# Performance work log

Measured on AMD Instinct MI355X. Metric: run time of the kernel, lower is better.

The kernel has to match this reference:

```python
import jax, jax.numpy as jnp
import numpy as np

N_EXPERTS = 8
TOPK = 2


def setup_inputs() -> dict:
    key = jax.random.key(0)
    k1, k2, k3, k4 = jax.random.split(key, 4)
    B, T, D, H, E = 2, 2048, 1024, 4096, N_EXPERTS
    s = 1.0 / np.sqrt(D)
    return {
        "x": jax.random.normal(k1, (B, T, D), dtype=jnp.float32),
        "W_gate": jax.random.normal(k2, (E, D), dtype=jnp.float32) * s,
        "W_fc": jax.random.normal(k3, (E, H, D), dtype=jnp.float32) * s,
        "W_proj": jax.random.normal(k4, (E, D, H), dtype=jnp.float32) * (1.0 / np.sqrt(H)),
    }


def reference(x, W_gate, W_fc, W_proj):
    B, T, D = x.shape
    E = W_gate.shape[0]
    N = B * T
    xf = x.reshape(N, D)

    # gating
    gate_logits = xf @ W_gate.T                       # [N, E]
    gate_probs = jax.nn.softmax(gate_logits, axis=-1)
    rw, eidx = jax.lax.top_k(gate_probs, TOPK)        # [N, K]
    rw = rw / jnp.sum(rw, axis=-1, keepdims=True)

    # exact dispatch: out[n] = sum_k rw[n,k] * MLP_{eidx[n,k]}(x[n])
    # loop over the small fixed expert count; each expert processes all tokens,
    # masked-combined by its per-token routing weight (same math as index_add dispatch).
    out = jnp.zeros_like(xf)
    for e in range(E):
        we = jnp.sum(jnp.where(eidx == e, rw, 0.0), axis=-1)     # [N]
        h = jnp.square(jax.nn.relu(xf @ W_fc[e].T))              # relu(x)^2, [N, H]
        out = out + (h @ W_proj[e].T) * we[:, None]

    # load-balance loss
    ones = jnp.ones((N * TOPK,), dtype=gate_probs.dtype)
    counts = jax.ops.segment_sum(ones, eidx.reshape(-1), num_segments=E)
    expert_freq = counts / N
    balance_loss = jnp.sum(gate_probs.mean(axis=0) * jax.lax.stop_gradient(expert_freq)) * E

    return out.reshape(B, T, D), balance_loss
```

## Files before the change

kernel.cpp:

```cpp
#include <hip/hip_runtime.h>
#include <hip/hip_bf16.h>
#include <math.h>

#define N_TOK 4096
#define D_DIM 1024
#define H_DIM 4096
#define E_NUM 8
#define NSLOT (N_TOK * 2)

typedef short bf16x8 __attribute__((ext_vector_type(8)));
typedef float f32x4 __attribute__((ext_vector_type(4)));


__device__ __forceinline__ unsigned short f2bf(float f) {
  unsigned int u = __float_as_uint(f);
  u += 0x7FFFu + ((u >> 16) & 1u);
  return (unsigned short)(u >> 16);
}

__device__ __forceinline__ void gld_lds16(const void* g, void* l) {
  __builtin_amdgcn_global_load_lds(
      (__attribute__((address_space(1))) void*)(g),
      (__attribute__((address_space(3))) void*)(l), 16, 0, 0);
}


__global__ void init_ctrl(int* p) { p[threadIdx.x] = 0; }

__global__ void cvt_f32_bf16(const float* __restrict__ src,
                             unsigned short* __restrict__ dst, int n4) {
  int i = blockIdx.x * blockDim.x + threadIdx.x;
  if (i >= n4) return;
  float4 v = ((const float4*)src)[i];
  ushort4 o;
  o.x = f2bf(v.x); o.y = f2bf(v.y); o.z = f2bf(v.z); o.w = f2bf(v.w);
  ((ushort4*)dst)[i] = o;
}

__global__ void zero_f32(float* __restrict__ p, int n4) {
  int i = blockIdx.x * blockDim.x + threadIdx.x;
  if (i < n4) ((float4*)p)[i] = make_float4(0.f, 0.f, 0.f, 0.f);
}


__global__ void gating_kernel(const float* __restrict__ x,
                              const float* __restrict__ wg,
                              float* __restrict__ probs,
                              int* __restrict__ eidx,
                              float* __restrict__ rw) {
  __shared__ float4 wg_lds[2048];
  const int t = threadIdx.x;
  const int lane = t & 63;
  const int wave = t >> 6;

#pragma unroll
  for (int j = 0; j < 8; ++j)
    wg_lds[t + 256 * j] = ((const float4*)wg)[t + 256 * j];
  __syncthreads();

#pragma unroll
  for (int j = 0; j < 4; ++j) {
    const int n = blockIdx.x * 16 + wave * 4 + j;
    const float4* xr = (const float4*)(x + (size_t)n * D_DIM);

    float acc[E_NUM];
#pragma unroll
    for (int e = 0; e < E_NUM; ++e) acc[e] = 0.f;

#pragma unroll
    for (int i = 0; i < 4; ++i) {
      float4 xv = xr[lane + 64 * i];
#pragma unroll
      for (int e = 0; e < E_NUM; ++e) {
        float4 wv = wg_lds[e * 256 + lane + 64 * i];
        acc[e] += xv.x * wv.x + xv.y * wv.y + xv.z * wv.z + xv.w * wv.w;
      }
    }
#pragma unroll
    for (int m = 1; m < 64; m <<= 1) {
#pragma unroll
      for (int e = 0; e < E_NUM; ++e) acc[e] += __shfl_xor(acc[e], m, 64);
    }

    float mx = acc[0];
#pragma unroll
    for (int e = 1; e < E_NUM; ++e) mx = fmaxf(mx, acc[e]);
    float p[E_NUM], s = 0.f;
#pragma unroll
    for (int e = 0; e < E_NUM; ++e) { p[e] = __expf(acc[e] - mx); s += p[e]; }
    float inv = 1.f / s;

    if (lane < E_NUM) probs[(size_t)n * E_NUM + lane] = p[lane] * inv;

    if (lane == 0) {
      int i1 = 0;
#pragma unroll
      for (int e = 1; e < E_NUM; ++e) if (p[e] > p[i1]) i1 = e;
      int i2 = (i1 == 0) ? 1 : 0;
#pragma unroll
      for (int e = 0; e < E_NUM; ++e)
        if (e != i1 && p[e] > p[i2]) i2 = e;
      float p1 = p[i1], p2 = p[i2];
      float wsum = 1.f / (p1 + p2);
      eidx[n] = i1 | (i2 << 8);
      rw[2 * n] = p1 * wsum;
      rw[2 * n + 1] = p2 * wsum;
    }
  }
}

__global__ void reduce_route(const float* __restrict__ probs,
                             const int* __restrict__ eidx,
                             int* __restrict__ counts,
                             int* __restrict__ offsets,
                             float* __restrict__ loss) {
  const int t = threadIdx.x;
  float4 part = make_float4(0.f, 0.f, 0.f, 0.f);
  for (int j = 0; j < 32; ++j) {
    float4 v = ((const float4*)probs)[t + 256 * j];
    part.x += v.x; part.y += v.y; part.z += v.z; part.w += v.w;
  }
  int cnt[E_NUM];
#pragma unroll
  for (int e = 0; e < E_NUM; ++e) cnt[e] = 0;
  for (int j = 0; j < 16; ++j) {
    int pk = eidx[t + 256 * j];
    int e1 = pk & 255, e2 = pk >> 8;
#pragma unroll
    for (int e = 0; e < E_NUM; ++e) cnt[e] += (e1 == e) + (e2 == e);
  }

  __shared__ float redf[256 * E_NUM];
  __shared__ int redi[256 * E_NUM];
  const int eb = (t & 1) * 4;
#pragma unroll
  for (int e = 0; e < E_NUM; ++e) { redf[t * E_NUM + e] = 0.f; redi[t * E_NUM + e] = cnt[e]; }
  redf[t * E_NUM + eb + 0] = part.x;
  redf[t * E_NUM + eb + 1] = part.y;
  redf[t * E_NUM + eb + 2] = part.z;
  redf[t * E_NUM + eb + 3] = part.w;
  __syncthreads();
  for (int s = 128; s > 0; s >>= 1) {
    if (t < s) {
#pragma unroll
      for (int e = 0; e < E_NUM; ++e) {
        redf[t * E_NUM + e] += redf[(t + s) * E_NUM + e];
        redi[t * E_NUM + e] += redi[(t + s) * E_NUM + e];
      }
    }
    __syncthreads();
  }
  if (t == 0) {
    int o = 0;
    float L = 0.f;
    for (int e = 0; e < E_NUM; ++e) {
      int c = redi[e];
      counts[e] = c;
      offsets[e] = o;
      o += c;
      L += redf[e] * (float)c;
    }
    loss[0] = L * (float)E_NUM / ((float)N_TOK * (float)N_TOK);
  }
}

__global__ void scatter_kernel(const int* __restrict__ eidx, const float* __restrict__ rw,
                               const int* __restrict__ offsets, int* __restrict__ cursor,
                               int* __restrict__ tok_id, float* __restrict__ tok_w) {
  __shared__ int lcnt[E_NUM];
  __shared__ int lbase[E_NUM];
  const int t = threadIdx.x;
  const int n = blockIdx.x * 256 + t;
  if (t < E_NUM) lcnt[t] = 0;
  __syncthreads();
  int pk = eidx[n];
  int e1 = pk & 255, e2 = pk >> 8;
  int p1 = atomicAdd(&lcnt[e1], 1);
  int p2 = atomicAdd(&lcnt[e2], 1);
  __syncthreads();
  if (t < E_NUM) lbase[t] = atomicAdd(&cursor[t], lcnt[t]);
  __syncthreads();
  int d1 = offsets[e1] + lbase[e1] + p1;
  tok_id[d1] = n; tok_w[d1] = rw[2 * n];
  int d2 = offsets[e2] + lbase[e2] + p2;
  tok_id[d2] = n; tok_w[d2] = rw[2 * n + 1];
}


__launch_bounds__(256, 2)
__global__ void gemm_fc(const unsigned short* __restrict__ xb,
                        const unsigned short* __restrict__ wfc,
                        const int* __restrict__ tok_id,
                        const int* __restrict__ counts,
                        const int* __restrict__ offsets,
                        unsigned short* __restrict__ hbuf) {
  const int e = blockIdx.z;
  const int cnt = counts[e];
  const int mtile = blockIdx.y;
  if (mtile * 128 >= cnt) return;
  const int ntile = blockIdx.x;
  const int off = offsets[e];

  __shared__ __align__(16) unsigned short As[128 * 64];
  __shared__ __align__(16) unsigned short Bs[128 * 64];

  const int t = threadIdx.x;
  const int lane = t & 63;
  const int wave = t >> 6;
  const int wm = (wave >> 1) * 64;
  const int wn = (wave & 1) * 64;
  const int srow = t >> 3;
  const int seg = (t & 7) ^ (srow & 7);

  const unsigned short* aptr[4];
  const unsigned short* bptr[4];
#pragma unroll
  for (int p = 0; p < 4; ++p) {
    int r = mtile * 128 + p * 32 + srow;
    r = (r < cnt) ? r : (cnt - 1);
    int tok = tok_id[off + r];
    aptr[p] = xb + (size_t)tok * D_DIM + seg * 8;
    int br = ntile * 128 + p * 32 + srow;
    bptr[p] = wfc + ((size_t)e * H_DIM + br) * D_DIM + seg * 8;
  }

  f32x4 acc[4][4];
#pragma unroll
  for (int i = 0; i < 4; ++i)
#pragma unroll
    for (int j = 0; j < 4; ++j) acc[i][j] = (f32x4){0.f, 0.f, 0.f, 0.f};

  const int frow_a = wm + (lane & 15);
  const int frow_b = wn + (lane & 15);
  const int q = lane >> 4;
  const int csw = lane & 7;

  for (int k0 = 0; k0 < D_DIM; k0 += 64) {
#pragma unroll
    for (int p = 0; p < 4; ++p) {
      gld_lds16(aptr[p] + k0, &As[p * 2048 + t * 8]);
      gld_lds16(bptr[p] + k0, &Bs[p * 2048 + t * 8]);
    }
    __syncthreads();
#pragma unroll
    for (int kk = 0; kk < 64; kk += 32) {
      const int ca = ((((kk >> 3) + q) ^ csw) << 3);
      bf16x8 af[4], bfr[4];
#pragma unroll
      for (int i = 0; i < 4; ++i)
        af[i] = *(const bf16x8*)&As[(frow_a + i * 16) * 64 + ca];
#pragma unroll
      for (int j = 0; j < 4; ++j)
        bfr[j] = *(const bf16x8*)&Bs[(frow_b + j * 16) * 64 + ca];
#pragma unroll
      for (int i = 0; i < 4; ++i)
#pragma unroll
        for (int j = 0; j < 4; ++j)
          acc[i][j] = __builtin_amdgcn_mfma_f32_16x16x32_bf16(af[i], bfr[j], acc[i][j], 0, 0, 0);
    }
    __syncthreads();
  }

  const int lm = (lane >> 4) * 4;
  const int ln = lane & 15;
#pragma unroll
  for (int i = 0; i < 4; ++i) {
#pragma unroll
    for (int r = 0; r < 4; ++r) {
      int m = mtile * 128 + wm + i * 16 + lm + r;
      if (m < cnt) {
        size_t rowbase = (size_t)(off + m) * H_DIM + ntile * 128 + wn;
#pragma unroll
        for (int j = 0; j < 4; ++j) {
          float v = acc[i][j][r];
          v = v > 0.f ? v * v : 0.f;
          hbuf[rowbase + j * 16 + ln] = f2bf(v);
        }
      }
    }
  }
}

__launch_bounds__(256, 2)
__global__ void gemm_proj(const unsigned short* __restrict__ hbuf,
                          const unsigned short* __restrict__ wproj,
                          const int* __restrict__ tok_id,
                          const float* __restrict__ tok_w,
                          const int* __restrict__ counts,
                          const int* __restrict__ offsets,
                          float* __restrict__ out) {
  const int e = blockIdx.z >> 1;
  const int kbase = (blockIdx.z & 1) * (H_DIM / 2);
  const int cnt = counts[e];
  const int mtile = blockIdx.y;
  if (mtile * 128 >= cnt) return;
  const int ntile = blockIdx.x;
  const int off = offsets[e];

  __shared__ __align__(16) unsigned short As[128 * 64];
  __shared__ __align__(16) unsigned short Bs[128 * 64];

  const int t = threadIdx.x;
  const int lane = t & 63;
  const int wave = t >> 6;
  const int wm = (wave >> 1) * 64;
  const int wn = (wave & 1) * 64;
  const int srow = t >> 3;
  const int seg = (t & 7) ^ (srow & 7);

  const unsigned short* aptr[4];
  const unsigned short* bptr[4];
#pragma unroll
  for (int p = 0; p < 4; ++p) {
    int r = mtile * 128 + p * 32 + srow;
    r = (r < cnt) ? r : (cnt - 1);
    aptr[p] = hbuf + (size_t)(off + r) * H_DIM + seg * 8;
    int br = ntile * 128 + p * 32 + srow;
    bptr[p] = wproj + ((size_t)e * D_DIM + br) * H_DIM + seg * 8;
  }

  f32x4 acc[4][4];
#pragma unroll
  for (int i = 0; i < 4; ++i)
#pragma unroll
    for (int j = 0; j < 4; ++j) acc[i][j] = (f32x4){0.f, 0.f, 0.f, 0.f};

  const int frow_a = wm + (lane & 15);
  const int frow_b = wn + (lane & 15);
  const int q = lane >> 4;
  const int csw = lane & 7;

  for (int k0 = kbase; k0 < kbase + H_DIM / 2; k0 += 64) {
#pragma unroll
    for (int p = 0; p < 4; ++p) {
      gld_lds16(aptr[p] + k0, &As[p * 2048 + t * 8]);
      gld_lds16(bptr[p] + k0, &Bs[p * 2048 + t * 8]);
    }
    __syncthreads();
#pragma unroll
    for (int kk = 0; kk < 64; kk += 32) {
      const int ca = ((((kk >> 3) + q) ^ csw) << 3);
      bf16x8 af[4], bfr[4];
#pragma unroll
      for (int i = 0; i < 4; ++i)
        af[i] = *(const bf16x8*)&As[(frow_a + i * 16) * 64 + ca];
#pragma unroll
      for (int j = 0; j < 4; ++j)
        bfr[j] = *(const bf16x8*)&Bs[(frow_b + j * 16) * 64 + ca];
#pragma unroll
      for (int i = 0; i < 4; ++i)
#pragma unroll
        for (int j = 0; j < 4; ++j)
          acc[i][j] = __builtin_amdgcn_mfma_f32_16x16x32_bf16(af[i], bfr[j], acc[i][j], 0, 0, 0);
    }
    __syncthreads();
  }

  const int lm = (lane >> 4) * 4;
  const int ln = lane & 15;
#pragma unroll
  for (int i = 0; i < 4; ++i) {
#pragma unroll
    for (int r = 0; r < 4; ++r) {
      int m = mtile * 128 + wm + i * 16 + lm + r;
      if (m < cnt) {
        int slot = off + m;
        float w = tok_w[slot];
        float* orow = out + (size_t)tok_id[slot] * D_DIM + ntile * 128 + wn;
#pragma unroll
        for (int j = 0; j < 4; ++j)
          atomicAdd(&orow[j * 16 + ln], acc[i][j][r] * w);
      }
    }
  }
}


extern "C" void kernel_launch(void* const* d_in, const int* in_sizes, int n_in,
                              void* d_out, int out_size, void* d_ws, size_t ws_size,
                              hipStream_t stream) {
  (void)in_sizes; (void)n_in; (void)out_size; (void)ws_size;
  const float* x = (const float*)d_in[0];
  const float* wg = (const float*)d_in[1];
  const float* wfc = (const float*)d_in[2];
  const float* wproj = (const float*)d_in[3];
  float* out = (float*)d_out;
  char* ws = (char*)d_ws;

  int* counts = (int*)(ws + 0);
  int* cursor = (int*)(ws + 64);
  int* offsets = (int*)(ws + 128);
  int* eidx = (int*)(ws + 256);
  float* rw = (float*)(ws + 16640);
  int* tok_id = (int*)(ws + 49408);
  float* tok_w = (float*)(ws + 82176);
  float* probs = (float*)(ws + 114944);
  unsigned short* xb = (unsigned short*)(ws + 246016);
  unsigned short* wfcb = (unsigned short*)(ws + 8634624);
  unsigned short* wpjb = (unsigned short*)(ws + 75743488);
  unsigned short* hbuf = (unsigned short*)(ws + 142852352);

  hipLaunchKernelGGL(init_ctrl, dim3(1), dim3(64), 0, stream, (int*)ws);
  hipLaunchKernelGGL(cvt_f32_bf16, dim3(32768), dim3(256), 0, stream, wfc, wfcb, 8388608);
  hipLaunchKernelGGL(cvt_f32_bf16, dim3(32768), dim3(256), 0, stream, wproj, wpjb, 8388608);
  hipLaunchKernelGGL(cvt_f32_bf16, dim3(4096), dim3(256), 0, stream, x, xb, 1048576);
  hipLaunchKernelGGL(zero_f32, dim3(4096), dim3(256), 0, stream, out, 1048576);
  hipLaunchKernelGGL(gating_kernel, dim3(256), dim3(256), 0, stream, x, wg, probs, eidx, rw);
  hipLaunchKernelGGL(reduce_route, dim3(1), dim3(256), 0, stream, probs, eidx, counts, offsets, out + 4194304);
  hipLaunchKernelGGL(scatter_kernel, dim3(16), dim3(256), 0, stream, eidx, rw, offsets, cursor, tok_id, tok_w);
  hipLaunchKernelGGL(gemm_fc, dim3(32, 32, 8), dim3(256), 0, stream, xb, wfcb, tok_id, counts, offsets, hbuf);
  hipLaunchKernelGGL(gemm_proj, dim3(8, 32, 16), dim3(256), 0, stream, hbuf, wpjb, tok_id, tok_w, counts, offsets, out);
}
```

Before: 563.2 us.

## Triple-buffer LDS pipeline with 256x128 tiles in expert GEMMs

```diff
diff --git a/kernel.cpp b/kernel.cpp
--- a/kernel.cpp
+++ b/kernel.cpp
@@ -187,7 +187,7 @@
 }
 
 
-__launch_bounds__(256, 2)
+__launch_bounds__(512, 2)
 __global__ void gemm_fc(const unsigned short* __restrict__ xb,
                         const unsigned short* __restrict__ wfc,
                         const int* __restrict__ tok_id,
@@ -197,32 +197,32 @@
   const int e = blockIdx.z;
   const int cnt = counts[e];
   const int mtile = blockIdx.y;
-  if (mtile * 128 >= cnt) return;
+  if (mtile * 256 >= cnt) return;
   const int ntile = blockIdx.x;
   const int off = offsets[e];
 
-  __shared__ __align__(16) unsigned short As[128 * 64];
-  __shared__ __align__(16) unsigned short Bs[128 * 64];
+  __shared__ __align__(16) unsigned short lds[3 * 24576];
 
   const int t = threadIdx.x;
   const int lane = t & 63;
   const int wave = t >> 6;
   const int wm = (wave >> 1) * 64;
   const int wn = (wave & 1) * 64;
+
   const int srow = t >> 3;
   const int seg = (t & 7) ^ (srow & 7);
 
   const unsigned short* aptr[4];
-  const unsigned short* bptr[4];
+  const unsigned short* bptr[2];
 #pragma unroll
   for (int p = 0; p < 4; ++p) {
-    int r = mtile * 128 + p * 32 + srow;
+    int r = mtile * 256 + p * 64 + srow;
     r = (r < cnt) ? r : (cnt - 1);
-    int tok = tok_id[off + r];
-    aptr[p] = xb + (size_t)tok * D_DIM + seg * 8;
-    int br = ntile * 128 + p * 32 + srow;
-    bptr[p] = wfc + ((size_t)e * H_DIM + br) * D_DIM + seg * 8;
-  }
+    aptr[p] = xb + (size_t)tok_id[off + r] * D_DIM + seg * 8;
+  }
+#pragma unroll
+  for (int p = 0; p < 2; ++p)
+    bptr[p] = wfc + ((size_t)e * H_DIM + ntile * 128 + p * 64 + srow) * D_DIM + seg * 8;
 
   f32x4 acc[4][4];
 #pragma unroll
@@ -230,58 +230,96 @@
 #pragma unroll
     for (int j = 0; j < 4; ++j) acc[i][j] = (f32x4){0.f, 0.f, 0.f, 0.f};
 
-  const int frow_a = wm + (lane & 15);
-  const int frow_b = wn + (lane & 15);
+  const int fr = lane & 15;
   const int q = lane >> 4;
   const int csw = lane & 7;
-
-  for (int k0 = 0; k0 < D_DIM; k0 += 64) {
-#pragma unroll
-    for (int p = 0; p < 4; ++p) {
-      gld_lds16(aptr[p] + k0, &As[p * 2048 + t * 8]);
-      gld_lds16(bptr[p] + k0, &Bs[p * 2048 + t * 8]);
-    }
-    __syncthreads();
-#pragma unroll
-    for (int kk = 0; kk < 64; kk += 32) {
-      const int ca = ((((kk >> 3) + q) ^ csw) << 3);
-      bf16x8 af[4], bfr[4];
-#pragma unroll
-      for (int i = 0; i < 4; ++i)
-        af[i] = *(const bf16x8*)&As[(frow_a + i * 16) * 64 + ca];
-#pragma unroll
-      for (int j = 0; j < 4; ++j)
-        bfr[j] = *(const bf16x8*)&Bs[(frow_b + j * 16) * 64 + ca];
-#pragma unroll
-      for (int i = 0; i < 4; ++i)
-#pragma unroll
-        for (int j = 0; j < 4; ++j)
-          acc[i][j] = __builtin_amdgcn_mfma_f32_16x16x32_bf16(af[i], bfr[j], acc[i][j], 0, 0, 0);
-    }
-    __syncthreads();
+  const int c0 = ((q ^ csw) << 3);
+  const int c1 = (((q + 4) ^ csw) << 3);
+
+  const int NK = D_DIM / 64;
+
+#pragma unroll
+  for (int p = 0; p < 4; ++p) gld_lds16(aptr[p], &lds[p * 4096 + t * 8]);
+#pragma unroll
+  for (int p = 0; p < 2; ++p) gld_lds16(bptr[p], &lds[16384 + p * 4096 + t * 8]);
+#pragma unroll
+  for (int p = 0; p < 4; ++p) gld_lds16(aptr[p] + 64, &lds[24576 + p * 4096 + t * 8]);
+#pragma unroll
+  for (int p = 0; p < 2; ++p) gld_lds16(bptr[p] + 64, &lds[24576 + 16384 + p * 4096 + t * 8]);
+  asm volatile("s_waitcnt vmcnt(6)" ::: "memory");
+  __builtin_amdgcn_s_barrier();
+
+  int sb = 0;
+  for (int kt = 0; kt < NK; ++kt) {
+    int stS = sb + 2 * 24576; if (stS >= 3 * 24576) stS -= 3 * 24576;
+    const unsigned short* Ab = &lds[sb + (wm + fr) * 64];
+    const unsigned short* Bb = &lds[sb + 16384 + (wn + fr) * 64];
+    const int kof = (kt + 2) * 64;
+    bf16x8 a_[4], b_[4];
+
+#pragma unroll
+    for (int m = 0; m < 4; ++m) a_[m] = *(const bf16x8*)(Ab + m * 1024 + c0);
+#pragma unroll
+    for (int n = 0; n < 4; ++n) b_[n] = *(const bf16x8*)(Bb + n * 1024 + c0);
+    if (kt + 2 < NK) {
+      gld_lds16(aptr[0] + kof, &lds[stS + t * 8]);
+      gld_lds16(aptr[1] + kof, &lds[stS + 4096 + t * 8]);
+      gld_lds16(aptr[2] + kof, &lds[stS + 8192 + t * 8]);
+    }
+    __builtin_amdgcn_s_barrier();
+    __builtin_amdgcn_s_setprio(1);
+#pragma unroll
+    for (int m = 0; m < 4; ++m)
+#pragma unroll
+      for (int n = 0; n < 4; ++n)
+        acc[m][n] = __builtin_amdgcn_mfma_f32_16x16x32_bf16(a_[m], b_[n], acc[m][n], 0, 0, 0);
+    __builtin_amdgcn_s_setprio(0);
+    __builtin_amdgcn_s_barrier();
+
+#pragma unroll
+    for (int m = 0; m < 4; ++m) a_[m] = *(const bf16x8*)(Ab + m * 1024 + c1);
+#pragma unroll
+    for (int n = 0; n < 4; ++n) b_[n] = *(const bf16x8*)(Bb + n * 1024 + c1);
+    if (kt + 2 < NK) {
+      gld_lds16(aptr[3] + kof, &lds[stS + 12288 + t * 8]);
+      gld_lds16(bptr[0] + kof, &lds[stS + 16384 + t * 8]);
+      gld_lds16(bptr[1] + kof, &lds[stS + 20480 + t * 8]);
+    }
+    __builtin_amdgcn_s_barrier();
+    __builtin_amdgcn_s_setprio(1);
+#pragma unroll
+    for (int m = 0; m < 4; ++m)
+#pragma unroll
+      for (int n = 0; n < 4; ++n)
+        acc[m][n] = __builtin_amdgcn_mfma_f32_16x16x32_bf16(a_[m], b_[n], acc[m][n], 0, 0, 0);
+    __builtin_amdgcn_s_setprio(0);
+    if (kt < NK - 2)       asm volatile("s_waitcnt vmcnt(6)" ::: "memory");
+    else if (kt == NK - 2) asm volatile("s_waitcnt vmcnt(0)" ::: "memory");
+    __builtin_amdgcn_s_barrier();
+    sb += 24576; if (sb >= 3 * 24576) sb = 0;
   }
 
   const int lm = (lane >> 4) * 4;
   const int ln = lane & 15;
 #pragma unroll
-  for (int i = 0; i < 4; ++i) {
+  for (int m = 0; m < 4; ++m) {
 #pragma unroll
     for (int r = 0; r < 4; ++r) {
-      int m = mtile * 128 + wm + i * 16 + lm + r;
-      if (m < cnt) {
-        size_t rowbase = (size_t)(off + m) * H_DIM + ntile * 128 + wn;
-#pragma unroll
-        for (int j = 0; j < 4; ++j) {
-          float v = acc[i][j][r];
+      int mm = mtile * 256 + wm + m * 16 + lm + r;
+      if (mm < cnt) {
+        size_t rowbase = (size_t)(off + mm) * H_DIM + ntile * 128 + wn;
+#pragma unroll
+        for (int n = 0; n < 4; ++n) {
+          float v = acc[m][n][r];
           v = v > 0.f ? v * v : 0.f;
-          hbuf[rowbase + j * 16 + ln] = f2bf(v);
+          hbuf[rowbase + n * 16 + ln] = f2bf(v);
         }
       }
     }
   }
 }
 
-__launch_bounds__(256, 2)
+__launch_bounds__(512, 2)
 __global__ void gemm_proj(const unsigned short* __restrict__ hbuf,
                           const unsigned short* __restrict__ wproj,
                           const int* __restrict__ tok_id,
@@ -293,31 +331,32 @@
   const int kbase = (blockIdx.z & 1) * (H_DIM / 2);
   const int cnt = counts[e];
   const int mtile = blockIdx.y;
-  if (mtile * 128 >= cnt) return;
+  if (mtile * 256 >= cnt) return;
   const int ntile = blockIdx.x;
   const int off = offsets[e];
 
-  __shared__ __align__(16) unsigned short As[128 * 64];
-  __shared__ __align__(16) unsigned short Bs[128 * 64];
+  __shared__ __align__(16) unsigned short lds[3 * 24576];
 
   const int t = threadIdx.x;
   const int lane = t & 63;
   const int wave = t >> 6;
   const int wm = (wave >> 1) * 64;
   const int wn = (wave & 1) * 64;
+
   const int srow = t >> 3;
   const int seg = (t & 7) ^ (srow & 7);
 
   const unsigned short* aptr[4];
-  const unsigned short* bptr[4];
+  const unsigned short* bptr[2];
 #pragma unroll
   for (int p = 0; p < 4; ++p) {
-    int r = mtile * 128 + p * 32 + srow;
+    int r = mtile * 256 + p * 64 + srow;
     r = (r < cnt) ? r : (cnt - 1);
-    aptr[p] = hbuf + (size_t)(off + r) * H_DIM + seg * 8;
-    int br = ntile * 128 + p * 32 + srow;
-    bptr[p] = wproj + ((size_t)e * D_DIM + br) * H_DIM + seg * 8;
-  }
+    aptr[p] = hbuf + (size_t)(off + r) * H_DIM + kbase + seg * 8;
+  }
+#pragma unroll
+  for (int p = 0; p < 2; ++p)
+    bptr[p] = wproj + ((size_t)e * D_DIM + ntile * 128 + p * 64 + srow) * H_DIM + kbase + seg * 8;
 
   f32x4 acc[4][4];
 #pragma unroll
@@ -325,51 +364,89 @@
 #pragma unroll
     for (int j = 0; j < 4; ++j) acc[i][j] = (f32x4){0.f, 0.f, 0.f, 0.f};
 
-  const int frow_a = wm + (lane & 15);
-  const int frow_b = wn + (lane & 15);
+  const int fr = lane & 15;
   const int q = lane >> 4;
   const int csw = lane & 7;
-
-  for (int k0 = kbase; k0 < kbase + H_DIM / 2; k0 += 64) {
-#pragma unroll
-    for (int p = 0; p < 4; ++p) {
-      gld_lds16(aptr[p] + k0, &As[p * 2048 + t * 8]);
-      gld_lds16(bptr[p] + k0, &Bs[p * 2048 + t * 8]);
-    }
-    __syncthreads();
-#pragma unroll
-    for (int kk = 0; kk < 64; kk += 32) {
-      const int ca = ((((kk >> 3) + q) ^ csw) << 3);
-      bf16x8 af[4], bfr[4];
-#pragma unroll
-      for (int i = 0; i < 4; ++i)
-        af[i] = *(const bf16x8*)&As[(frow_a + i * 16) * 64 + ca];
-#pragma unroll
-      for (int j = 0; j < 4; ++j)
-        bfr[j] = *(const bf16x8*)&Bs[(frow_b + j * 16) * 64 + ca];
-#pragma unroll
-      for (int i = 0; i < 4; ++i)
-#pragma unroll
-        for (int j = 0; j < 4; ++j)
-          acc[i][j] = __builtin_amdgcn_mfma_f32_16x16x32_bf16(af[i], bfr[j], acc[i][j], 0, 0, 0);
-    }
-    __syncthreads();
+  const int c0 = ((q ^ csw) << 3);
+  const int c1 = (((q + 4) ^ csw) << 3);
+
+  const int NK = (H_DIM / 2) / 64;
+
+#pragma unroll
+  for (int p = 0; p < 4; ++p) gld_lds16(aptr[p], &lds[p * 4096 + t * 8]);
+#pragma unroll
+  for (int p = 0; p < 2; ++p) gld_lds16(bptr[p], &lds[16384 + p * 4096 + t * 8]);
+#pragma unroll
+  for (int p = 0; p < 4; ++p) gld_lds16(aptr[p] + 64, &lds[24576 + p * 4096 + t * 8]);
+#pragma unroll
+  for (int p = 0; p < 2; ++p) gld_lds16(bptr[p] + 64, &lds[24576 + 16384 + p * 4096 + t * 8]);
+  asm volatile("s_waitcnt vmcnt(6)" ::: "memory");
+  __builtin_amdgcn_s_barrier();
+
+  int sb = 0;
+  for (int kt = 0; kt < NK; ++kt) {
+    int stS = sb + 2 * 24576; if (stS >= 3 * 24576) stS -= 3 * 24576;
+    const unsigned short* Ab = &lds[sb + (wm + fr) * 64];
+    const unsigned short* Bb = &lds[sb + 16384 + (wn + fr) * 64];
+    const int kof = (kt + 2) * 64;
+    bf16x8 a_[4], b_[4];
+
+#pragma unroll
+    for (int m = 0; m < 4; ++m) a_[m] = *(const bf16x8*)(Ab + m * 1024 + c0);
+#pragma unroll
+    for (int n = 0; n < 4; ++n) b_[n] = *(const bf16x8*)(Bb + n * 1024 + c0);
+    if (kt + 2 < NK) {
+      gld_lds16(aptr[0] + kof, &lds[stS + t * 8]);
+      gld_lds16(aptr[1] + kof, &lds[stS + 4096 + t * 8]);
+      gld_lds16(aptr[2] + kof, &lds[stS + 8192 + t * 8]);
+    }
+    __builtin_amdgcn_s_barrier();
+    __builtin_amdgcn_s_setprio(1);
+#pragma unroll
+    for (int m = 0; m < 4; ++m)
+#pragma unroll
+      for (int n = 0; n < 4; ++n)
+        acc[m][n] = __builtin_amdgcn_mfma_f32_16x16x32_bf16(a_[m], b_[n], acc[m][n], 0, 0, 0);
+    __builtin_amdgcn_s_setprio(0);
+    __builtin_amdgcn_s_barrier();
+
+#pragma unroll
+    for (int m = 0; m < 4; ++m) a_[m] = *(const bf16x8*)(Ab + m * 1024 + c1);
+#pragma unroll
+    for (int n = 0; n < 4; ++n) b_[n] = *(const bf16x8*)(Bb + n * 1024 + c1);
+    if (kt + 2 < NK) {
+      gld_lds16(aptr[3] + kof, &lds[stS + 12288 + t * 8]);
+      gld_lds16(bptr[0] + kof, &lds[stS + 16384 + t * 8]);
+      gld_lds16(bptr[1] + kof, &lds[stS + 20480 + t * 8]);
+    }
+    __builtin_amdgcn_s_barrier();
+    __builtin_amdgcn_s_setprio(1);
+#pragma unroll
+    for (int m = 0; m < 4; ++m)
+#pragma unroll
+      for (int n = 0; n < 4; ++n)
+        acc[m][n] = __builtin_amdgcn_mfma_f32_16x16x32_bf16(a_[m], b_[n], acc[m][n], 0, 0, 0);
+    __builtin_amdgcn_s_setprio(0);
+    if (kt < NK - 2)       asm volatile("s_waitcnt vmcnt(6)" ::: "memory");
+    else if (kt == NK - 2) asm volatile("s_waitcnt vmcnt(0)" ::: "memory");
+    __builtin_amdgcn_s_barrier();
+    sb += 24576; if (sb >= 3 * 24576) sb = 0;
   }
 
   const int lm = (lane >> 4) * 4;
   const int ln = lane & 15;
 #pragma unroll
-  for (int i = 0; i < 4; ++i) {
+  for (int m = 0; m < 4; ++m) {
 #pragma unroll
     for (int r = 0; r < 4; ++r) {
-      int m = mtile * 128 + wm + i * 16 + lm + r;
-      if (m < cnt) {
-        int slot = off + m;
+      int mm = mtile * 256 + wm + m * 16 + lm + r;
+      if (mm < cnt) {
+        int slot = off + mm;
         float w = tok_w[slot];
         float* orow = out + (size_t)tok_id[slot] * D_DIM + ntile * 128 + wn;
 #pragma unroll
-        for (int j = 0; j < 4; ++j)
-          atomicAdd(&orow[j * 16 + ln], acc[i][j][r] * w);
+        for (int n = 0; n < 4; ++n)
+          atomicAdd(&orow[n * 16 + ln], acc[m][n][r] * w);
       }
     }
   }
@@ -408,6 +485,6 @@
   hipLaunchKernelGGL(gating_kernel, dim3(256), dim3(256), 0, stream, x, wg, probs, eidx, rw);
   hipLaunchKernelGGL(reduce_route, dim3(1), dim3(256), 0, stream, probs, eidx, counts, offsets, out + 4194304);
   hipLaunchKernelGGL(scatter_kernel, dim3(16), dim3(256), 0, stream, eidx, rw, offsets, cursor, tok_id, tok_w);
-  hipLaunchKernelGGL(gemm_fc, dim3(32, 32, 8), dim3(256), 0, stream, xb, wfcb, tok_id, counts, offsets, hbuf);
-  hipLaunchKernelGGL(gemm_proj, dim3(8, 32, 16), dim3(256), 0, stream, hbuf, wpjb, tok_id, tok_w, counts, offsets, out);
-}
+  hipLaunchKernelGGL(gemm_fc, dim3(32, 16, 8), dim3(512), 0, stream, xb, wfcb, tok_id, counts, offsets, hbuf);
+  hipLaunchKernelGGL(gemm_proj, dim3(8, 16, 16), dim3(512), 0, stream, hbuf, wpjb, tok_id, tok_w, counts, offsets, out);
+}
```

Measured after the change: 571.1 us. About the same (+1.4%).

## Pipeline expert GEMMs with a 4-stage LDS ring and async prefetch

Applied to the files above, without the earlier changes.

```diff
diff --git a/kernel.cpp b/kernel.cpp
--- a/kernel.cpp
+++ b/kernel.cpp
@@ -187,6 +187,11 @@
 }
 
 
+#define BK 32
+#define RING 4
+#define BUFSZ 8192
+#define SRC_CHUNK(s) ((((s) & 3) ^ (((s) >> 3) & 3)) * 8)
+
 __launch_bounds__(256, 2)
 __global__ void gemm_fc(const unsigned short* __restrict__ xb,
                         const unsigned short* __restrict__ wfc,
@@ -196,33 +201,26 @@
                         unsigned short* __restrict__ hbuf) {
   const int e = blockIdx.z;
   const int cnt = counts[e];
-  const int mtile = blockIdx.y;
+  const int mtile = blockIdx.x;
   if (mtile * 128 >= cnt) return;
-  const int ntile = blockIdx.x;
+  const int ntile = blockIdx.y;
   const int off = offsets[e];
 
-  __shared__ __align__(16) unsigned short As[128 * 64];
-  __shared__ __align__(16) unsigned short Bs[128 * 64];
+  __shared__ __align__(16) unsigned short lds[RING * BUFSZ];
 
   const int t = threadIdx.x;
   const int lane = t & 63;
   const int wave = t >> 6;
   const int wm = (wave >> 1) * 64;
   const int wn = (wave & 1) * 64;
-  const int srow = t >> 3;
-  const int seg = (t & 7) ^ (srow & 7);
-
-  const unsigned short* aptr[4];
-  const unsigned short* bptr[4];
-#pragma unroll
-  for (int p = 0; p < 4; ++p) {
-    int r = mtile * 128 + p * 32 + srow;
-    r = (r < cnt) ? r : (cnt - 1);
-    int tok = tok_id[off + r];
-    aptr[p] = xb + (size_t)tok * D_DIM + seg * 8;
-    int br = ntile * 128 + p * 32 + srow;
-    bptr[p] = wfc + ((size_t)e * H_DIM + br) * D_DIM + seg * 8;
-  }
+
+  const int s0 = t, s1 = t + 256;
+  int r0 = mtile * 128 + (s0 >> 2); r0 = (r0 < cnt) ? r0 : (cnt - 1);
+  int r1 = mtile * 128 + (s1 >> 2); r1 = (r1 < cnt) ? r1 : (cnt - 1);
+  const unsigned short* ga0 = xb + (size_t)tok_id[off + r0] * D_DIM + SRC_CHUNK(s0);
+  const unsigned short* ga1 = xb + (size_t)tok_id[off + r1] * D_DIM + SRC_CHUNK(s1);
+  const unsigned short* gb0 = wfc + ((size_t)e * H_DIM + ntile * 128 + (s0 >> 2)) * D_DIM + SRC_CHUNK(s0);
+  const unsigned short* gb1 = wfc + ((size_t)e * H_DIM + ntile * 128 + (s1 >> 2)) * D_DIM + SRC_CHUNK(s1);
 
   f32x4 acc[4][4];
 #pragma unroll
@@ -230,35 +228,54 @@
 #pragma unroll
     for (int j = 0; j < 4; ++j) acc[i][j] = (f32x4){0.f, 0.f, 0.f, 0.f};
 
-  const int frow_a = wm + (lane & 15);
-  const int frow_b = wn + (lane & 15);
+  const int fr = lane & 15;
   const int q = lane >> 4;
-  const int csw = lane & 7;
-
-  for (int k0 = 0; k0 < D_DIM; k0 += 64) {
-#pragma unroll
-    for (int p = 0; p < 4; ++p) {
-      gld_lds16(aptr[p] + k0, &As[p * 2048 + t * 8]);
-      gld_lds16(bptr[p] + k0, &Bs[p * 2048 + t * 8]);
-    }
-    __syncthreads();
-#pragma unroll
-    for (int kk = 0; kk < 64; kk += 32) {
-      const int ca = ((((kk >> 3) + q) ^ csw) << 3);
-      bf16x8 af[4], bfr[4];
-#pragma unroll
-      for (int i = 0; i < 4; ++i)
-        af[i] = *(const bf16x8*)&As[(frow_a + i * 16) * 64 + ca];
+  const int ch = (q ^ ((fr >> 1) & 3)) * 8;
+
+  const int NK = D_DIM / BK;
+
+#pragma unroll
+  for (int p = 0; p < 3; ++p) {
+    gld_lds16(ga0 + p * BK, &lds[p * BUFSZ + t * 8]);
+    gld_lds16(ga1 + p * BK, &lds[p * BUFSZ + 2048 + t * 8]);
+    gld_lds16(gb0 + p * BK, &lds[p * BUFSZ + 4096 + t * 8]);
+    gld_lds16(gb1 + p * BK, &lds[p * BUFSZ + 4096 + 2048 + t * 8]);
+  }
+  asm volatile("s_waitcnt vmcnt(8)" ::: "memory");
+  __builtin_amdgcn_s_barrier();
+
+  for (int kt = 0; kt < NK; ++kt) {
+    const int bb = (kt & 3) * BUFSZ;
+    const unsigned short* Ab = &lds[bb + (wm + fr) * 32 + ch];
+    const unsigned short* Bb = &lds[bb + 4096 + (wn + fr) * 32 + ch];
+
+    bf16x8 a_[4], b_[4];
+#pragma unroll
+    for (int i = 0; i < 4; ++i) a_[i] = *(const bf16x8*)(Ab + i * 512);
+#pragma unroll
+    for (int j = 0; j < 4; ++j) b_[j] = *(const bf16x8*)(Bb + j * 512);
+
+    if (kt + 3 < NK) {
+      const int kof = (kt + 3) * BK;
+      const int sb = ((kt + 3) & 3) * BUFSZ;
+      gld_lds16(ga0 + kof, &lds[sb + t * 8]);
+      gld_lds16(ga1 + kof, &lds[sb + 2048 + t * 8]);
+      gld_lds16(gb0 + kof, &lds[sb + 4096 + t * 8]);
+      gld_lds16(gb1 + kof, &lds[sb + 4096 + 2048 + t * 8]);
+    }
+
+    __builtin_amdgcn_s_setprio(1);
+#pragma unroll
+    for (int i = 0; i < 4; ++i)
 #pragma unroll
       for (int j = 0; j < 4; ++j)
-        bfr[j] = *(const bf16x8*)&Bs[(frow_b + j * 16) * 64 + ca];
-#pragma unroll
-      for (int i = 0; i < 4; ++i)
-#pragma unroll
-        for (int j = 0; j < 4; ++j)
-          acc[i][j] = __builtin_amdgcn_mfma_f32_16x16x32_bf16(af[i], bfr[j], acc[i][j], 0, 0, 0);
-    }
-    __syncthreads();
+        acc[i][j] = __builtin_amdgcn_mfma_f32_16x16x32_bf16(a_[i], b_[j], acc[i][j], 0, 0, 0);
+    __builtin_amdgcn_s_setprio(0);
+
+    if (kt < NK - 3)       asm volatile("s_waitcnt vmcnt(8)" ::: "memory");
+    else if (kt == NK - 3) asm volatile("s_waitcnt vmcnt(4)" ::: "memory");
+    else if (kt == NK - 2) asm volatile("s_waitcnt vmcnt(0)" ::: "memory");
+    if (kt != NK - 1) __builtin_amdgcn_s_barrier();
   }
 
   const int lm = (lane >> 4) * 4;
@@ -292,32 +309,26 @@
   const int e = blockIdx.z >> 1;
   const int kbase = (blockIdx.z & 1) * (H_DIM / 2);
   const int cnt = counts[e];
-  const int mtile = blockIdx.y;
+  const int mtile = blockIdx.x;
   if (mtile * 128 >= cnt) return;
-  const int ntile = blockIdx.x;
+  const int ntile = blockIdx.y;
   const int off = offsets[e];
 
-  __shared__ __align__(16) unsigned short As[128 * 64];
-  __shared__ __align__(16) unsigned short Bs[128 * 64];
+  __shared__ __align__(16) unsigned short lds[RING * BUFSZ];
 
   const int t = threadIdx.x;
   const int lane = t & 63;
   const int wave = t >> 6;
   const int wm = (wave >> 1) * 64;
   const int wn = (wave & 1) * 64;
-  const int srow = t >> 3;
-  const int seg = (t & 7) ^ (srow & 7);
-
-  const unsigned short* aptr[4];
-  const unsigned short* bptr[4];
-#pragma unroll
-  for (int p = 0; p < 4; ++p) {
-    int r = mtile * 128 + p * 32 + srow;
-    r = (r < cnt) ? r : (cnt - 1);
-    aptr[p] = hbuf + (size_t)(off + r) * H_DIM + seg * 8;
-    int br = ntile * 128 + p * 32 + srow;
-    bptr[p] = wproj + ((size_t)e * D_DIM + br) * H_DIM + seg * 8;
-  }
+
+  const int s0 = t, s1 = t + 256;
+  int r0 = mtile * 128 + (s0 >> 2); r0 = (r0 < cnt) ? r0 : (cnt - 1);
+  int r1 = mtile * 128 + (s1 >> 2); r1 = (r1 < cnt) ? r1 : (cnt - 1);
+  const unsigned short* ga0 = hbuf + (size_t)(off + r0) * H_DIM + kbase + SRC_CHUNK(s0);
+  const unsigned short* ga1 = hbuf + (size_t)(off + r1) * H_DIM + kbase + SRC_CHUNK(s1);
+  const unsigned short* gb0 = wproj + ((size_t)e * D_DIM + ntile * 128 + (s0 >> 2)) * H_DIM + kbase + SRC_CHUNK(s0);
+  const unsigned short* gb1 = wproj + ((size_t)e * D_DIM + ntile * 128 + (s1 >> 2)) * H_DIM + kbase + SRC_CHUNK(s1);
 
   f32x4 acc[4][4];
 #pragma unroll
@@ -325,35 +336,54 @@
 #pragma unroll
     for (int j = 0; j < 4; ++j) acc[i][j] = (f32x4){0.f, 0.f, 0.f, 0.f};
 
-  const int frow_a = wm + (lane & 15);
-  const int frow_b = wn + (lane & 15);
+  const int fr = lane & 15;
   const int q = lane >> 4;
-  const int csw = lane & 7;
-
-  for (int k0 = kbase; k0 < kbase + H_DIM / 2; k0 += 64) {
-#pragma unroll
-    for (int p = 0; p < 4; ++p) {
-      gld_lds16(aptr[p] + k0, &As[p * 2048 + t * 8]);
-      gld_lds16(bptr[p] + k0, &Bs[p * 2048 + t * 8]);
-    }
-    __syncthreads();
-#pragma unroll
-    for (int kk = 0; kk < 64; kk += 32) {
-      const int ca = ((((kk >> 3) + q) ^ csw) << 3);
-      bf16x8 af[4], bfr[4];
-#pragma unroll
-      for (int i = 0; i < 4; ++i)
-        af[i] = *(const bf16x8*)&As[(frow_a + i * 16) * 64 + ca];
+  const int ch = (q ^ ((fr >> 1) & 3)) * 8;
+
+  const int NK = (H_DIM / 2) / BK;
+
+#pragma unroll
+  for (int p = 0; p < 3; ++p) {
+    gld_lds16(ga0 + p * BK, &lds[p * BUFSZ + t * 8]);
+    gld_lds16(ga1 + p * BK, &lds[p * BUFSZ + 2048 + t * 8]);
+    gld_lds16(gb0 + p * BK, &lds[p * BUFSZ + 4096 + t * 8]);
+    gld_lds16(gb1 + p * BK, &lds[p * BUFSZ + 4096 + 2048 + t * 8]);
+  }
+  asm volatile("s_waitcnt vmcnt(8)" ::: "memory");
+  __builtin_amdgcn_s_barrier();
+
+  for (int kt = 0; kt < NK; ++kt) {
+    const int bb = (kt & 3) * BUFSZ;
+    const unsigned short* Ab = &lds[bb + (wm + fr) * 32 + ch];
+    const unsigned short* Bb = &lds[bb + 4096 + (wn + fr) * 32 + ch];
+
+    bf16x8 a_[4], b_[4];
+#pragma unroll
+    for (int i = 0; i < 4; ++i) a_[i] = *(const bf16x8*)(Ab + i * 512);
+#pragma unroll
+    for (int j = 0; j < 4; ++j) b_[j] = *(const bf16x8*)(Bb + j * 512);
+
+    if (kt + 3 < NK) {
+      const int kof = (kt + 3) * BK;
+      const int sb = ((kt + 3) & 3) * BUFSZ;
+      gld_lds16(ga0 + kof, &lds[sb + t * 8]);
+      gld_lds16(ga1 + kof, &lds[sb + 2048 + t * 8]);
+      gld_lds16(gb0 + kof, &lds[sb + 4096 + t * 8]);
+      gld_lds16(gb1 + kof, &lds[sb + 4096 + 2048 + t * 8]);
+    }
+
+    __builtin_amdgcn_s_setprio(1);
+#pragma unroll
+    for (int i = 0; i < 4; ++i)
 #pragma unroll
       for (int j = 0; j < 4; ++j)
-        bfr[j] = *(const bf16x8*)&Bs[(frow_b + j * 16) * 64 + ca];
-#pragma unroll
-      for (int i = 0; i < 4; ++i)
-#pragma unroll
-        for (int j = 0; j < 4; ++j)
-          acc[i][j] = __builtin_amdgcn_mfma_f32_16x16x32_bf16(af[i], bfr[j], acc[i][j], 0, 0, 0);
-    }
-    __syncthreads();
+        acc[i][j] = __builtin_amdgcn_mfma_f32_16x16x32_bf16(a_[i], b_[j], acc[i][j], 0, 0, 0);
+    __builtin_amdgcn_s_setprio(0);
+
+    if (kt < NK - 3)       asm volatile("s_waitcnt vmcnt(8)" ::: "memory");
+    else if (kt == NK - 3) asm volatile("s_waitcnt vmcnt(4)" ::: "memory");
+    else if (kt == NK - 2) asm volatile("s_waitcnt vmcnt(0)" ::: "memory");
+    if (kt != NK - 1) __builtin_amdgcn_s_barrier();
   }
 
   const int lm = (lane >> 4) * 4;
@@ -409,5 +439,5 @@
   hipLaunchKernelGGL(reduce_route, dim3(1), dim3(256), 0, stream, probs, eidx, counts, offsets, out + 4194304);
   hipLaunchKernelGGL(scatter_kernel, dim3(16), dim3(256), 0, stream, eidx, rw, offsets, cursor, tok_id, tok_w);
   hipLaunchKernelGGL(gemm_fc, dim3(32, 32, 8), dim3(256), 0, stream, xb, wfcb, tok_id, counts, offsets, hbuf);
-  hipLaunchKernelGGL(gemm_proj, dim3(8, 32, 16), dim3(256), 0, stream, hbuf, wpjb, tok_id, tok_w, counts, offsets, out);
-}
+  hipLaunchKernelGGL(gemm_proj, dim3(32, 8, 16), dim3(256), 0, stream, hbuf, wpjb, tok_id, tok_w, counts, offsets, out);
+}
```

Result: slower. 979.3 us (+73.9%).
